# Optimization experiments

Hardware: AMD Instinct MI355X
Metric: run time of the kernel (lower is better)

The kernel has to match this reference:

```python
import jax, jax.numpy as jnp
import numpy as np

PATCH = 256
N = 50000
HC = 256  # height // PATCH
WC = 256  # width // PATCH

def _gauss_kernel():
    # GaussianSmoothing(channels=1, kernel_size=3, sigma=0.5)
    g = np.exp(-(((np.arange(3, dtype=np.float64) - 1.0) / 0.5) ** 2) / 2.0) / (0.5 * np.sqrt(2 * np.pi))
    k = np.outer(g, g)
    k = k / k.sum()
    return jnp.asarray(k, jnp.float32).reshape(1, 1, 3, 3)

def setup_inputs() -> dict:
    key = jax.random.key(0)
    ks = jax.random.split(key, 12)
    h = jax.random.normal(ks[0], (N, 1024), jnp.float32)
    # unique grid cells per patch (row-major), scaled back to pixel coords
    idx = jnp.arange(N, dtype=jnp.int64 if jax.config.jax_enable_x64 else jnp.int32)
    gx = idx % WC
    gy = idx // WC
    coords = jnp.stack([gx * PATCH, gy * PATCH], axis=1)
    eps = jax.random.normal(ks[1], (1, 1, HC, WC), jnp.float32)
    s = 0.02
    W1 = jax.random.normal(ks[2], (512, 1024), jnp.float32) * s
    b1 = jnp.zeros((512,), jnp.float32)
    W2a = jax.random.normal(ks[3], (256, 512), jnp.float32) * s
    b2a = jnp.zeros((256,), jnp.float32)
    W2b = jax.random.normal(ks[4], (256, 512), jnp.float32) * s
    b2b = jnp.zeros((256,), jnp.float32)
    W3 = jax.random.normal(ks[5], (2, 256), jnp.float32) * s
    b3 = jnp.zeros((2,), jnp.float32)
    Wc = jax.random.normal(ks[6], (2, 512), jnp.float32) * s
    bc = jnp.zeros((2,), jnp.float32)
    kernel = _gauss_kernel()
    return {"h": h, "coords": coords, "eps": eps,
            "W1": W1, "b1": b1, "W2a": W2a, "b2a": b2a, "W2b": W2b, "b2b": b2b,
            "W3": W3, "b3": b3, "Wc": Wc, "bc": bc, "kernel": kernel,
            "height": 65536, "width": 65536, "slide_label": 1}

def reference(h, coords, eps, W1, b1, W2a, b2a, W2b, b2b, W3, b3, Wc, bc, kernel, height, width, slide_label):
    hc, wc = height // PATCH, width // PATCH
    x = jax.nn.relu(h @ W1.T + b1)                      # [N,512] (dropout = eval identity)
    fa = jax.nn.sigmoid(x @ W2a.T + b2a)                # [N,256]
    fb = jnp.tanh(x @ W2b.T + b2b)                      # [N,256]
    params = (fa * fb) @ W3.T + b3                      # [N,2] -> (mu, logvar) per patch
    gx = coords[:, 0] // PATCH
    gy = coords[:, 1] // PATCH
    mu = jnp.zeros((1, hc, wc), x.dtype).at[0, gy, gx].set(params[:, 0])
    logvar = jnp.zeros((1, hc, wc), x.dtype).at[0, gy, gx].set(params[:, 1])
    prior_mu = jnp.array([-5.0, 0.0], x.dtype)[slide_label]
    prior_lv = jnp.array([-1.0, 3.0], x.dtype)[slide_label]
    kl_div = (prior_lv - logvar) / 2.0 + (logvar ** 2 + (prior_mu - mu) ** 2) / (2.0 * prior_lv ** 2) - 0.5
    mu_pad = jnp.pad(mu, ((0, 0), (1, 1), (1, 1)))[None]          # [1,1,hc+2,wc+2]
    mu_sm = jax.lax.conv_general_dilated(mu_pad, kernel, (1, 1), 'VALID')  # [1,1,hc,wc]
    samples = mu_sm + eps * jnp.exp(0.5 * logvar)                  # reparameterize, broadcast to [1,1,hc,wc]
    A = jax.nn.sigmoid(samples[0])                                 # [1,hc,wc]
    patch_A = A[0, gy, gx][None]                                   # gather -> [1,N]
    M = (patch_A @ x) / patch_A.sum()                              # [1,512]
    logits = M @ Wc.T + bc                                         # [1,n_classes]
    y_probs = jax.nn.softmax(logits, axis=1)
    top_idx = jax.lax.top_k(y_probs[:, 1], 1)[1]                   # top_k=1
    top_instance = logits[top_idx]                                 # [1,n_classes]
    Y_hat = jnp.argmax(top_instance, axis=1, keepdims=True)
    Y_prob = jax.nn.softmax(top_instance, axis=1)
    return (top_instance, Y_prob, Y_hat, kl_div, y_probs, patch_A)
```

## Files before the change

kernel.cpp:

```cpp
#include <hip/hip_runtime.h>
#include <hip/hip_bf16.h>
#include <cstdint>
#include <cstddef>

#define NPATCH 50000
#define GC 256

typedef __bf16 bf16x8 __attribute__((ext_vector_type(8)));
typedef float  f32x4  __attribute__((ext_vector_type(4)));
typedef float  f32x8  __attribute__((ext_vector_type(8)));

static constexpr size_t XB_OFF    = 0;
static constexpr size_t XB_BYTES  = (size_t)50048 * 512 * 2;
static constexpr size_t W1B_OFF   = XB_OFF + XB_BYTES;
static constexpr size_t W1B_BYTES = (size_t)512 * 1024 * 2;
static constexpr size_t W2AB_OFF  = W1B_OFF + W1B_BYTES;
static constexpr size_t W2X_BYTES = (size_t)256 * 512 * 2;
static constexpr size_t W2BB_OFF  = W2AB_OFF + W2X_BYTES;
static constexpr size_t MUG_OFF   = W2BB_OFF + W2X_BYTES;
static constexpr size_t LVG_OFF   = MUG_OFF + (size_t)65536 * 4;
static constexpr size_t AG_OFF    = LVG_OFF + (size_t)65536 * 4;
static constexpr size_t MPART_OFF = AG_OFF + (size_t)65536 * 4;
static constexpr size_t SUMA_OFF  = MPART_OFF + (size_t)512 * 4;
static constexpr size_t ZERO_BYTES = SUMA_OFF + 4 - MUG_OFF;
static constexpr int    ZERO_F32   = (int)(ZERO_BYTES / 4);

__device__ __forceinline__ unsigned short f2bf(float f) {
  union { float f; uint32_t u; } v; v.f = f;
  uint32_t u = v.u;
  uint32_t r = (u + 0x7FFFu + ((u >> 16) & 1u)) >> 16;
  return (unsigned short)r;
}
__device__ __forceinline__ float bf2f(uint32_t bits16) {
  union { uint32_t u; float f; } v; v.u = bits16 << 16; return v.f;
}
__device__ __forceinline__ unsigned short cvt_bf16(float f) {
  __bf16 b = (__bf16)f;
  return __builtin_bit_cast(unsigned short, b);
}
__device__ __forceinline__ void gld16(const void* g, void* l) {
  __builtin_amdgcn_global_load_lds(
      (const __attribute__((address_space(1))) void*)g,
      (__attribute__((address_space(3))) void*)l, 16, 0, 0);
}
__device__ __forceinline__ bf16x8 cvt8(const float4& f0, const float4& f1) {
  f32x8 fv;
  fv[0]=f0.x; fv[1]=f0.y; fv[2]=f0.z; fv[3]=f0.w;
  fv[4]=f1.x; fv[5]=f1.y; fv[6]=f1.z; fv[7]=f1.w;
  return __builtin_convertvector(fv, bf16x8);
}

__global__ void convert_weights(const float* __restrict__ W1,
                                const float* __restrict__ W2a,
                                const float* __restrict__ W2b,
                                unsigned short* __restrict__ W1b,
                                unsigned short* __restrict__ W2ab,
                                unsigned short* __restrict__ W2bb,
                                float* __restrict__ zws) {
  int i = blockIdx.x * 256 + threadIdx.x;
  if (i < 512 * 1024) W1b[i] = f2bf(W1[i]);
  if (i < 256 * 512) { W2ab[i] = f2bf(W2a[i]); W2bb[i] = f2bf(W2b[i]); }
  if (i < ZERO_F32) zws[i] = 0.f;
}

__global__ __launch_bounds__(512, 2) void gemm1(
    const float* __restrict__ h, const unsigned short* __restrict__ W1b,
    const float* __restrict__ b1, unsigned short* __restrict__ xb) {
  __shared__ __align__(16) unsigned short lds[40960];
  unsigned short* const A0 = lds;
  unsigned short* const A1 = lds + 8192;
  unsigned short* const B0 = lds + 16384;
  unsigned short* const B1 = lds + 24576;
  unsigned short* const B2 = lds + 32768;

  const int t  = threadIdx.x;
  const int l  = t & 63;
  const int w  = t >> 6;
  const int wm = w >> 2;
  const int wn = w & 3;
  const int g  = l >> 4;
  const int lr = l & 15;

  const int i   = blockIdx.x;
  const int xcd = i & 7;
  const int pos = i >> 3;
  const int v   = xcd * 49 + pos;
  const int rt  = v >> 1;
  const int ct  = v & 1;
  const int rowBase = rt * 256;
  const int colBase = ct * 256;

  const int tr = t >> 1;
  const int hh = t & 1;
  int gr = rowBase + tr; if (gr >= NPATCH) gr = NPATCH - 1;
  const float* ah = h + (size_t)gr * 1024 + hh * 16;
  const int sw  = (tr >> 1) & 3;
  const int aw0 = tr * 32 + ((hh * 2)     ^ sw) * 8;
  const int aw1 = tr * 32 + ((hh * 2 + 1) ^ sw) * 8;

  const int bj = (t & 3) ^ ((t >> 3) & 3);
  const unsigned short* bh  = W1b + (size_t)(colBase + (t >> 2)) * 1024 + bj * 8;
  const unsigned short* bh2 = bh + (size_t)128 * 1024;
  const int bd0 = t * 8;
  const int bd1 = 4096 + t * 8;

  const int rs = (g ^ ((lr >> 1) & 3)) * 8;
  const int abase = (wm * 128 + lr) * 32 + rs;
  const int bbase = (wn * 64 + lr) * 32 + rs;

  f32x4 acc[8][4];
#pragma unroll
  for (int m = 0; m < 8; ++m)
#pragma unroll
    for (int n = 0; n < 4; ++n) acc[m][n] = (f32x4){0.f, 0.f, 0.f, 0.f};

  unsigned short *pAr = A0, *pAw = A1;
  unsigned short *pBr = B0, *pBr1 = B1, *pBw = B2;

  float4 q0, q1, q2, q3;
  {
    gld16(bh, pBr + bd0); gld16(bh2, pBr + bd1);
    float4 f0 = *(const float4*)(ah + 0);
    float4 f1 = *(const float4*)(ah + 4);
    float4 f2 = *(const float4*)(ah + 8);
    float4 f3 = *(const float4*)(ah + 12);
    *(bf16x8*)(pAr + aw0) = cvt8(f0, f1);
    *(bf16x8*)(pAr + aw1) = cvt8(f2, f3);
    q0 = *(const float4*)(ah + 32);
    q1 = *(const float4*)(ah + 36);
    q2 = *(const float4*)(ah + 40);
    q3 = *(const float4*)(ah + 44);
    gld16(bh + 32, pBr1 + bd0); gld16(bh2 + 32, pBr1 + bd1);
  }
  asm volatile("s_waitcnt lgkmcnt(0)\n\ts_barrier" ::: "memory");

  for (int kt = 0; kt < 32; ++kt) {
    const int ka = ((kt + 2 <= 31) ? (kt + 2) : 31) * 32;
    bf16x8 af[4], bf[4];
#pragma unroll
    for (int m = 0; m < 4; ++m)
      af[m] = *(const bf16x8*)(pAr + abase + m * 512);
#pragma unroll
    for (int n = 0; n < 4; ++n)
      bf[n] = *(const bf16x8*)(pBr + bbase + n * 512);
    gld16(bh + ka, pBw + bd0);
    gld16(bh2 + ka, pBw + bd1);
    __builtin_amdgcn_sched_barrier(0);
    __builtin_amdgcn_s_barrier();
    __builtin_amdgcn_s_setprio(1);
#pragma unroll
    for (int m = 0; m < 4; ++m)
#pragma unroll
      for (int n = 0; n < 4; ++n)
        acc[m][n] = __builtin_amdgcn_mfma_f32_16x16x32_bf16(af[m], bf[n], acc[m][n], 0, 0, 0);
    __builtin_amdgcn_s_setprio(0);
    __builtin_amdgcn_s_barrier();
#pragma unroll
    for (int m = 0; m < 4; ++m)
      af[m] = *(const bf16x8*)(pAr + abase + (m + 4) * 512);
    *(bf16x8*)(pAw + aw0) = cvt8(q0, q1);
    *(bf16x8*)(pAw + aw1) = cvt8(q2, q3);
    q0 = *(const float4*)(ah + ka + 0);
    q1 = *(const float4*)(ah + ka + 4);
    q2 = *(const float4*)(ah + ka + 8);
    q3 = *(const float4*)(ah + ka + 12);
    __builtin_amdgcn_sched_barrier(0);
    __builtin_amdgcn_s_barrier();
    __builtin_amdgcn_s_setprio(1);
#pragma unroll
    for (int m = 0; m < 4; ++m)
#pragma unroll
      for (int n = 0; n < 4; ++n)
        acc[m + 4][n] = __builtin_amdgcn_mfma_f32_16x16x32_bf16(af[m], bf[n], acc[m + 4][n], 0, 0, 0);
    __builtin_amdgcn_s_setprio(0);
    asm volatile("s_waitcnt vmcnt(6) lgkmcnt(0)\n\ts_barrier" ::: "memory");
    unsigned short* tA = pAr; pAr = pAw; pAw = tA;
    unsigned short* tB = pBr; pBr = pBr1; pBr1 = pBw; pBw = tB;
  }
  asm volatile("s_waitcnt vmcnt(0) lgkmcnt(0)" ::: "memory");

  float b1v[4];
#pragma unroll
  for (int n = 0; n < 4; ++n) b1v[n] = b1[colBase + wn * 64 + n * 16 + lr];
#pragma unroll
  for (int m = 0; m < 8; ++m) {
    const int rb0 = rowBase + wm * 128 + m * 16 + g * 4;
#pragma unroll
    for (int r = 0; r < 4; ++r) {
      const int row = rb0 + r;
      if (row < NPATCH) {
        unsigned short* xrow = xb + (size_t)row * 512 + colBase + wn * 64;
#pragma unroll
        for (int n = 0; n < 4; ++n) {
          float vv = acc[m][n][r] + b1v[n];
          vv = vv > 0.f ? vv : 0.f;
          xrow[n * 16 + lr] = cvt_bf16(vv);
        }
      }
    }
  }
}

__global__ __launch_bounds__(512) void gemm2(
    const unsigned short* __restrict__ xb,
    const unsigned short* __restrict__ W2ab, const unsigned short* __restrict__ W2bb,
    const float* __restrict__ b2a, const float* __restrict__ b2b,
    const float* __restrict__ W3, const float* __restrict__ b3,
    const int* __restrict__ coords,
    float* __restrict__ mug, float* __restrict__ lvg) {
  __shared__ __align__(16) unsigned short xs[2][128 * 32];
  __shared__ __align__(16) unsigned short was[2][256 * 32];
  __shared__ __align__(16) unsigned short wbs[2][256 * 32];
  __shared__ float pmu_s[4][128];
  __shared__ float plv_s[4][128];

  const int t  = threadIdx.x;
  const int l  = t & 63;
  const int w  = t >> 6;
  const int wm = w >> 2;
  const int wn = w & 3;
  const int g  = l >> 4;
  const int lr = l & 15;
  const int rowBase = blockIdx.x * 128;

  const int bj = (t & 3) ^ ((t >> 3) & 3);
  const unsigned short* xsrc   = xb   + (size_t)(rowBase + (t >> 2)) * 512 + bj * 8;
  const unsigned short* wasrc0 = W2ab + (size_t)(t >> 2) * 512 + bj * 8;
  const unsigned short* wasrc1 = wasrc0 + (size_t)128 * 512;
  const unsigned short* wbsrc0 = W2bb + (size_t)(t >> 2) * 512 + bj * 8;
  const unsigned short* wbsrc1 = wbsrc0 + (size_t)128 * 512;
  const int d0 = t * 8;
  const int d1 = 4096 + t * 8;

  const int rslot = (g ^ ((lr >> 1) & 3)) * 8;

  f32x4 aa[4][4], ab[4][4];
#pragma unroll
  for (int m = 0; m < 4; ++m)
#pragma unroll
    for (int n = 0; n < 4; ++n) {
      aa[m][n] = (f32x4){0.f, 0.f, 0.f, 0.f};
      ab[m][n] = (f32x4){0.f, 0.f, 0.f, 0.f};
    }

  {
    gld16(xsrc,   &xs[0][d0]);
    gld16(wasrc0, &was[0][d0]);
    gld16(wasrc1, &was[0][d1]);
    gld16(wbsrc0, &wbs[0][d0]);
    gld16(wbsrc1, &wbs[0][d1]);
  }
  __syncthreads();

  int cur = 0;
  for (int kt = 0; kt < 16; ++kt) {
    if (kt < 15) {
      const int k0 = (kt + 1) * 32;
      gld16(xsrc + k0,   &xs[cur ^ 1][d0]);
      gld16(wasrc0 + k0, &was[cur ^ 1][d0]);
      gld16(wasrc1 + k0, &was[cur ^ 1][d1]);
      gld16(wbsrc0 + k0, &wbs[cur ^ 1][d0]);
      gld16(wbsrc1 + k0, &wbs[cur ^ 1][d1]);
    }
    bf16x8 af[4], ba[4], bb[4];
#pragma unroll
    for (int m = 0; m < 4; ++m)
      af[m] = *(const bf16x8*)&xs[cur][(wm * 64 + m * 16 + lr) * 32 + rslot];
#pragma unroll
    for (int n = 0; n < 4; ++n) {
      const int brow = (wn * 64 + n * 16 + lr) * 32 + rslot;
      ba[n] = *(const bf16x8*)&was[cur][brow];
      bb[n] = *(const bf16x8*)&wbs[cur][brow];
    }
#pragma unroll
    for (int m = 0; m < 4; ++m)
#pragma unroll
      for (int n = 0; n < 4; ++n) {
        aa[m][n] = __builtin_amdgcn_mfma_f32_16x16x32_bf16(af[m], ba[n], aa[m][n], 0, 0, 0);
        ab[m][n] = __builtin_amdgcn_mfma_f32_16x16x32_bf16(af[m], bb[n], ab[m][n], 0, 0, 0);
      }
    __syncthreads();
    cur ^= 1;
  }

  float b2av[4], b2bv[4], w30v[4], w31v[4];
#pragma unroll
  for (int n = 0; n < 4; ++n) {
    const int col = wn * 64 + n * 16 + lr;
    b2av[n] = b2a[col]; b2bv[n] = b2b[col];
    w30v[n] = W3[col];  w31v[n] = W3[256 + col];
  }
#pragma unroll
  for (int m = 0; m < 4; ++m) {
#pragma unroll
    for (int r = 0; r < 4; ++r) {
      float pm = 0.f, pl = 0.f;
#pragma unroll
      for (int n = 0; n < 4; ++n) {
        float a = 1.f / (1.f + __expf(-(aa[m][n][r] + b2av[n])));
        float b = tanhf(ab[m][n][r] + b2bv[n]);
        float p = a * b;
        pm += p * w30v[n];
        pl += p * w31v[n];
      }
#pragma unroll
      for (int d = 1; d < 16; d <<= 1) {
        pm += __shfl_xor(pm, d, 64);
        pl += __shfl_xor(pl, d, 64);
      }
      if (lr == 0) {
        pmu_s[wn][wm * 64 + m * 16 + g * 4 + r] = pm;
        plv_s[wn][wm * 64 + m * 16 + g * 4 + r] = pl;
      }
    }
  }
  __syncthreads();
  if (t < 128) {
    float mu = pmu_s[0][t] + pmu_s[1][t] + pmu_s[2][t] + pmu_s[3][t] + b3[0];
    float lv = plv_s[0][t] + plv_s[1][t] + plv_s[2][t] + plv_s[3][t] + b3[1];
    int row = rowBase + t;
    if (row < NPATCH) {
      int gx = coords[2 * row] >> 8;
      int gy = coords[2 * row + 1] >> 8;
      int cell = gy * GC + gx;
      mug[cell] = mu;
      lvg[cell] = lv;
    }
  }
}

__global__ void grid_ops(const float* __restrict__ mug, const float* __restrict__ lvg,
                         const float* __restrict__ eps, const float* __restrict__ kern,
                         const int* __restrict__ slide, float* __restrict__ Ag,
                         float* __restrict__ out_kl) {
  int cell = blockIdx.x * 256 + threadIdx.x;
  int iy = cell >> 8, ix = cell & 255;
  float mu = mug[cell], lv = lvg[cell];
  int sl = slide[0];
  float pm  = (sl == 0) ? -5.0f : 0.0f;
  float plv = (sl == 0) ? -1.0f : 3.0f;
  float d = pm - mu;
  out_kl[cell] = (plv - lv) * 0.5f + (lv * lv + d * d) / (2.0f * plv * plv) - 0.5f;
  float s = 0.f;
#pragma unroll
  for (int dy = 0; dy < 3; ++dy) {
#pragma unroll
    for (int dx = 0; dx < 3; ++dx) {
      int y = iy + dy - 1, x = ix + dx - 1;
      if (y >= 0 && y < GC && x >= 0 && x < GC)
        s += mug[y * GC + x] * kern[dy * 3 + dx];
    }
  }
  float sample = s + eps[cell] * __expf(0.5f * lv);
  Ag[cell] = 1.f / (1.f + __expf(-sample));
}

__global__ __launch_bounds__(256) void patch_pass(
    const float* __restrict__ Ag, const int* __restrict__ coords,
    const unsigned short* __restrict__ xb, float* __restrict__ out_pA,
    float* __restrict__ Mpart, float* __restrict__ sumA) {
  __shared__ float als[256];
  __shared__ float swave[4];
  const int t = threadIdx.x;
  const int base = blockIdx.x * 256;
  const int row = base + t;
  float a = 0.f;
  if (row < NPATCH) {
    int gx = coords[2 * row] >> 8;
    int gy = coords[2 * row + 1] >> 8;
    a = Ag[gy * GC + gx];
    out_pA[row] = a;
  }
  als[t] = a;
  float sa = a;
#pragma unroll
  for (int d = 1; d < 64; d <<= 1) sa += __shfl_xor(sa, d, 64);
  if ((t & 63) == 0) swave[t >> 6] = sa;
  __syncthreads();
  if (t == 0) atomicAdd(sumA, swave[0] + swave[1] + swave[2] + swave[3]);

  const int nrows = min(256, NPATCH - base);
  float m0 = 0.f, m1 = 0.f;
  for (int r = 0; r < nrows; ++r) {
    float av = als[r];
    const uint32_t* p = (const uint32_t*)(xb + (size_t)(base + r) * 512);
    uint32_t v = p[t];
    m0 += av * bf2f(v & 0xFFFFu);
    m1 += av * bf2f(v >> 16);
  }
  atomicAdd(&Mpart[t * 2 + 0], m0);
  atomicAdd(&Mpart[t * 2 + 1], m1);
}

__global__ void finalize(const float* __restrict__ Mpart, const float* __restrict__ sumA,
                         const float* __restrict__ Wc, const float* __restrict__ bc,
                         float* __restrict__ out) {
  const int t = threadIdx.x;
  float s = sumA[0];
  float l0 = 0.f, l1 = 0.f;
#pragma unroll
  for (int j = 0; j < 8; ++j) {
    int c = t * 8 + j;
    float m = Mpart[c] / s;
    l0 += m * Wc[c];
    l1 += m * Wc[512 + c];
  }
#pragma unroll
  for (int d = 1; d < 64; d <<= 1) {
    l0 += __shfl_xor(l0, d, 64);
    l1 += __shfl_xor(l1, d, 64);
  }
  if (t == 0) {
    l0 += bc[0]; l1 += bc[1];
    float mx = fmaxf(l0, l1);
    float e0 = __expf(l0 - mx), e1 = __expf(l1 - mx);
    float inv = 1.f / (e0 + e1);
    float p0 = e0 * inv, p1 = e1 * inv;
    out[0] = l0; out[1] = l1;
    out[2] = p0; out[3] = p1;
    out[4] = (l1 > l0) ? 1.0f : 0.0f;
    out[65541] = p0; out[65542] = p1;
  }
}

extern "C" void kernel_launch(void* const* d_in, const int* in_sizes, int n_in,
                              void* d_out, int out_size, void* d_ws, size_t ws_size,
                              hipStream_t stream) {
  const float* h      = (const float*)d_in[0];
  const int*   coords = (const int*)d_in[1];
  const float* eps    = (const float*)d_in[2];
  const float* W1     = (const float*)d_in[3];
  const float* b1     = (const float*)d_in[4];
  const float* W2a    = (const float*)d_in[5];
  const float* b2a    = (const float*)d_in[6];
  const float* W2b    = (const float*)d_in[7];
  const float* b2b    = (const float*)d_in[8];
  const float* W3     = (const float*)d_in[9];
  const float* b3     = (const float*)d_in[10];
  const float* Wc     = (const float*)d_in[11];
  const float* bc     = (const float*)d_in[12];
  const float* kern   = (const float*)d_in[13];
  const int*   slide  = (const int*)d_in[16];
  float* out = (float*)d_out;
  char*  ws  = (char*)d_ws;

  unsigned short* xb   = (unsigned short*)(ws + XB_OFF);
  unsigned short* W1b  = (unsigned short*)(ws + W1B_OFF);
  unsigned short* W2ab = (unsigned short*)(ws + W2AB_OFF);
  unsigned short* W2bb = (unsigned short*)(ws + W2BB_OFF);
  float* mug   = (float*)(ws + MUG_OFF);
  float* lvg   = (float*)(ws + LVG_OFF);
  float* Ag    = (float*)(ws + AG_OFF);
  float* Mpart = (float*)(ws + MPART_OFF);
  float* sumA  = (float*)(ws + SUMA_OFF);

  convert_weights<<<2048, 256, 0, stream>>>(W1, W2a, W2b, W1b, W2ab, W2bb,
                                            (float*)(ws + MUG_OFF));
  gemm1<<<392, 512, 0, stream>>>(h, W1b, b1, xb);
  gemm2<<<391, 512, 0, stream>>>(xb, W2ab, W2bb, b2a, b2b, W3, b3, coords, mug, lvg);
  grid_ops<<<256, 256, 0, stream>>>(mug, lvg, eps, kern, slide, Ag, out + 5);
  patch_pass<<<196, 256, 0, stream>>>(Ag, coords, xb, out + 65543, Mpart, sumA);
  finalize<<<1, 64, 0, stream>>>(Mpart, sumA, Wc, bc, out);
}
```

Before: 188.3 us.

## Reorder gemm1 loads and replace atomics with per-block partials in patch reduction

The gemm1 main loop now issues the A-tile convert/store and the next global float4 loads before the first MFMA half. The B-tile global-to-LDS loads move after it, which changes how memory traffic overlaps compute. The patch pass now uses 392 blocks of 128 rows instead of 196 blocks of 256. Each block writes its partial M vector and A-sum to a workspace slot instead of using global atomics. A 256-thread finalize kernel then sums the 392 partials serially per column, which adds serial reads to a single-block kernel.

After: 183.4 us. -2.6%, faster.

```diff
diff --git a/kernel.cpp b/kernel.cpp
--- a/kernel.cpp
+++ b/kernel.cpp
@@ -24,6 +24,8 @@
 static constexpr size_t SUMA_OFF  = MPART_OFF + (size_t)512 * 4;
 static constexpr size_t ZERO_BYTES = SUMA_OFF + 4 - MUG_OFF;
 static constexpr int    ZERO_F32   = (int)(ZERO_BYTES / 4);
+static constexpr size_t MPART2_OFF = ((SUMA_OFF + 4 + 63) / 64) * 64;
+static constexpr size_t SUMAP_OFF  = MPART2_OFF + (size_t)392 * 512 * 4;
 
 __device__ __forceinline__ unsigned short f2bf(float f) {
   union { float f; uint32_t u; } v; v.f = f;
@@ -143,27 +145,27 @@
 #pragma unroll
     for (int n = 0; n < 4; ++n)
       bf[n] = *(const bf16x8*)(pBr + bbase + n * 512);
-    gld16(bh + ka, pBw + bd0);
-    gld16(bh2 + ka, pBw + bd1);
-    __builtin_amdgcn_sched_barrier(0);
-    __builtin_amdgcn_s_barrier();
-    __builtin_amdgcn_s_setprio(1);
-#pragma unroll
-    for (int m = 0; m < 4; ++m)
-#pragma unroll
-      for (int n = 0; n < 4; ++n)
-        acc[m][n] = __builtin_amdgcn_mfma_f32_16x16x32_bf16(af[m], bf[n], acc[m][n], 0, 0, 0);
-    __builtin_amdgcn_s_setprio(0);
-    __builtin_amdgcn_s_barrier();
-#pragma unroll
-    for (int m = 0; m < 4; ++m)
-      af[m] = *(const bf16x8*)(pAr + abase + (m + 4) * 512);
     *(bf16x8*)(pAw + aw0) = cvt8(q0, q1);
     *(bf16x8*)(pAw + aw1) = cvt8(q2, q3);
     q0 = *(const float4*)(ah + ka + 0);
     q1 = *(const float4*)(ah + ka + 4);
     q2 = *(const float4*)(ah + ka + 8);
     q3 = *(const float4*)(ah + ka + 12);
+    __builtin_amdgcn_sched_barrier(0);
+    __builtin_amdgcn_s_barrier();
+    __builtin_amdgcn_s_setprio(1);
+#pragma unroll
+    for (int m = 0; m < 4; ++m)
+#pragma unroll
+      for (int n = 0; n < 4; ++n)
+        acc[m][n] = __builtin_amdgcn_mfma_f32_16x16x32_bf16(af[m], bf[n], acc[m][n], 0, 0, 0);
+    __builtin_amdgcn_s_setprio(0);
+    __builtin_amdgcn_s_barrier();
+#pragma unroll
+    for (int m = 0; m < 4; ++m)
+      af[m] = *(const bf16x8*)(pAr + abase + (m + 4) * 512);
+    gld16(bh + ka, pBw + bd0);
+    gld16(bh2 + ka, pBw + bd1);
     __builtin_amdgcn_sched_barrier(0);
     __builtin_amdgcn_s_barrier();
     __builtin_amdgcn_s_setprio(1);
@@ -358,60 +360,75 @@
 __global__ __launch_bounds__(256) void patch_pass(
     const float* __restrict__ Ag, const int* __restrict__ coords,
     const unsigned short* __restrict__ xb, float* __restrict__ out_pA,
-    float* __restrict__ Mpart, float* __restrict__ sumA) {
-  __shared__ float als[256];
-  __shared__ float swave[4];
+    float* __restrict__ Mpart2, float* __restrict__ sumAp) {
+  __shared__ float als[128];
+  __shared__ float sred[2];
   const int t = threadIdx.x;
-  const int base = blockIdx.x * 256;
-  const int row = base + t;
-  float a = 0.f;
-  if (row < NPATCH) {
-    int gx = coords[2 * row] >> 8;
-    int gy = coords[2 * row + 1] >> 8;
-    a = Ag[gy * GC + gx];
-    out_pA[row] = a;
-  }
-  als[t] = a;
-  float sa = a;
-#pragma unroll
-  for (int d = 1; d < 64; d <<= 1) sa += __shfl_xor(sa, d, 64);
-  if ((t & 63) == 0) swave[t >> 6] = sa;
+  const int base = blockIdx.x * 128;
+
+  if (t < 128) {
+    const int row = base + t;
+    float a = 0.f;
+    if (row < NPATCH) {
+      int gx = coords[2 * row] >> 8;
+      int gy = coords[2 * row + 1] >> 8;
+      a = Ag[gy * GC + gx];
+      out_pA[row] = a;
+    }
+    als[t] = a;
+    float sa = a;
+#pragma unroll
+    for (int d = 1; d < 64; d <<= 1) sa += __shfl_xor(sa, d, 64);
+    if ((t & 63) == 0) sred[t >> 6] = sa;
+  }
   __syncthreads();
-  if (t == 0) atomicAdd(sumA, swave[0] + swave[1] + swave[2] + swave[3]);
-
-  const int nrows = min(256, NPATCH - base);
+  if (t == 0) sumAp[blockIdx.x] = sred[0] + sred[1];
+
+  int nrows = NPATCH - base;
+  if (nrows > 128) nrows = 128;
+  if (nrows < 0) nrows = 0;
   float m0 = 0.f, m1 = 0.f;
   for (int r = 0; r < nrows; ++r) {
-    float av = als[r];
-    const uint32_t* p = (const uint32_t*)(xb + (size_t)(base + r) * 512);
-    uint32_t v = p[t];
+    const float av = als[r];
+    const uint32_t v = *(const uint32_t*)(xb + (size_t)(base + r) * 512 + t * 2);
     m0 += av * bf2f(v & 0xFFFFu);
     m1 += av * bf2f(v >> 16);
   }
-  atomicAdd(&Mpart[t * 2 + 0], m0);
-  atomicAdd(&Mpart[t * 2 + 1], m1);
-}
-
-__global__ void finalize(const float* __restrict__ Mpart, const float* __restrict__ sumA,
-                         const float* __restrict__ Wc, const float* __restrict__ bc,
-                         float* __restrict__ out) {
+  Mpart2[(size_t)blockIdx.x * 512 + 2 * t]     = m0;
+  Mpart2[(size_t)blockIdx.x * 512 + 2 * t + 1] = m1;
+}
+
+__global__ __launch_bounds__(256) void finalize(
+    const float* __restrict__ Mpart2, const float* __restrict__ sumAp,
+    const float* __restrict__ Wc, const float* __restrict__ bc,
+    float* __restrict__ out) {
+  __shared__ float red0[4], red1[4], reds[4];
   const int t = threadIdx.x;
-  float s = sumA[0];
-  float l0 = 0.f, l1 = 0.f;
-#pragma unroll
-  for (int j = 0; j < 8; ++j) {
-    int c = t * 8 + j;
-    float m = Mpart[c] / s;
-    l0 += m * Wc[c];
-    l1 += m * Wc[512 + c];
-  }
+  const int c0 = 2 * t, c1 = 2 * t + 1;
+  float m0 = 0.f, m1 = 0.f;
+  for (int b = 0; b < 392; ++b) {
+    m0 += Mpart2[(size_t)b * 512 + c0];
+    m1 += Mpart2[(size_t)b * 512 + c1];
+  }
+  float sa = 0.f;
+  if (t < 196) sa = sumAp[t] + ((t + 196 < 392) ? sumAp[t + 196] : 0.f);
+#pragma unroll
+  for (int d = 1; d < 64; d <<= 1) sa += __shfl_xor(sa, d, 64);
+  if ((t & 63) == 0) reds[t >> 6] = sa;
+
+  float l0 = m0 * Wc[c0] + m1 * Wc[c1];
+  float l1 = m0 * Wc[512 + c0] + m1 * Wc[512 + c1];
 #pragma unroll
   for (int d = 1; d < 64; d <<= 1) {
     l0 += __shfl_xor(l0, d, 64);
     l1 += __shfl_xor(l1, d, 64);
   }
+  if ((t & 63) == 0) { red0[t >> 6] = l0; red1[t >> 6] = l1; }
+  __syncthreads();
   if (t == 0) {
-    l0 += bc[0]; l1 += bc[1];
+    const float s = reds[0] + reds[1] + reds[2] + reds[3];
+    l0 = (red0[0] + red0[1] + red0[2] + red0[3]) / s + bc[0];
+    l1 = (red1[0] + red1[1] + red1[2] + red1[3]) / s + bc[1];
     float mx = fmaxf(l0, l1);
     float e0 = __expf(l0 - mx), e1 = __expf(l1 - mx);
     float inv = 1.f / (e0 + e1);
@@ -448,17 +465,17 @@
   unsigned short* W1b  = (unsigned short*)(ws + W1B_OFF);
   unsigned short* W2ab = (unsigned short*)(ws + W2AB_OFF);
   unsigned short* W2bb = (unsigned short*)(ws + W2BB_OFF);
-  float* mug   = (float*)(ws + MUG_OFF);
-  float* lvg   = (float*)(ws + LVG_OFF);
-  float* Ag    = (float*)(ws + AG_OFF);
-  float* Mpart = (float*)(ws + MPART_OFF);
-  float* sumA  = (float*)(ws + SUMA_OFF);
+  float* mug    = (float*)(ws + MUG_OFF);
+  float* lvg    = (float*)(ws + LVG_OFF);
+  float* Ag     = (float*)(ws + AG_OFF);
+  float* Mpart2 = (float*)(ws + MPART2_OFF);
+  float* sumAp  = (float*)(ws + SUMAP_OFF);
 
   convert_weights<<<2048, 256, 0, stream>>>(W1, W2a, W2b, W1b, W2ab, W2bb,
                                             (float*)(ws + MUG_OFF));
   gemm1<<<392, 512, 0, stream>>>(h, W1b, b1, xb);
   gemm2<<<391, 512, 0, stream>>>(xb, W2ab, W2bb, b2a, b2b, W3, b3, coords, mug, lvg);
   grid_ops<<<256, 256, 0, stream>>>(mug, lvg, eps, kern, slide, Ag, out + 5);
-  patch_pass<<<196, 256, 0, stream>>>(Ag, coords, xb, out + 65543, Mpart, sumA);
-  finalize<<<1, 64, 0, stream>>>(Mpart, sumA, Wc, bc, out);
-}
+  patch_pass<<<392, 256, 0, stream>>>(Ag, coords, xb, out + 65543, Mpart2, sumAp);
+  finalize<<<1, 256, 0, stream>>>(Mpart2, sumAp, Wc, bc, out);
+}
```
